# Performance work log

Measured on AMD Instinct MI355X. Metric: run time of the kernel, lower is better.

## Reference

```python
import jax, jax.numpy as jnp
import numpy as np

B = 16
Dv, Hv, Wv = 128, 128, 128   # patchsize voxel grid (C=1)
NPTS = 1920                  # 16*120 points
EPS_IN = 1e-5                # InstanceNorm eps


def _inorm(x):
    # InstanceNorm1d, affine=False: normalize over last (length) dim per (b, c)
    m = jnp.mean(x, axis=-1, keepdims=True)
    v = jnp.var(x, axis=-1, keepdims=True)
    return (x - m) * jax.lax.rsqrt(v + EPS_IN)


def _mlp(q, w1, b1, w2, b2, w3, b3, w4, b4, w5, b5):
    b = q.shape[0]
    x = q.reshape(b, 256, 8)                                    # (b, 2048//8, 8)
    x = jnp.einsum('bil,oi->bol', x, w1) + b1[None, :, None]    # Conv1d(256,240,1) -> (b,240,8)
    x = jax.nn.relu(_inorm(x.reshape(b, 64, 30)))               # view (b,64,30), IN(64)
    # Conv1d(64,128,1,groups=64): each in-ch -> 2 out-chs; then view (b,32,120)
    x = (x[:, :, None, :] * w2[None, :, :, None] + b2.reshape(1, 64, 2, 1)).reshape(b, 32, 120)
    x = jax.nn.relu(_inorm(x))
    # Conv1d(32,64,1,groups=32); view (b,16,480)
    x = (x[:, :, None, :] * w3[None, :, :, None] + b3.reshape(1, 32, 2, 1)).reshape(b, 16, 480)
    x = jax.nn.relu(_inorm(x))
    # Conv1d(16,64,1,groups=16); view (b,16,1920)
    x = (x[:, :, None, :] * w4[None, :, :, None] + b4.reshape(1, 16, 4, 1)).reshape(b, 16, 1920)
    x = jax.nn.relu(_inorm(x))
    return jnp.einsum('bil,oi->bol', x, w5) + b5[None, :, None]  # Conv1d(16,3,1) -> (b,3,1920)


def _splat(vals, grid):
    # True adjoint of 3D grid_sample (align_corners=False, zeros padding):
    # trilinear scatter-add of point values into the voxel grid.
    # vals: (b, N); grid: (b, N, 3) with (x, y, z) ~ (W, H, D) normalized coords.
    b, n = vals.shape
    px = ((grid[..., 0] + 1.0) * Wv - 1.0) * 0.5
    py = ((grid[..., 1] + 1.0) * Hv - 1.0) * 0.5
    pz = ((grid[..., 2] + 1.0) * Dv - 1.0) * 0.5
    x0f = jnp.floor(px); y0f = jnp.floor(py); z0f = jnp.floor(pz)
    fx = px - x0f; fy = py - y0f; fz = pz - z0f
    x0 = x0f.astype(jnp.int32); y0 = y0f.astype(jnp.int32); z0 = z0f.astype(jnp.int32)
    bidx = jnp.arange(b, dtype=jnp.int32)[:, None]
    out = jnp.zeros(b * Dv * Hv * Wv, dtype=vals.dtype)
    for dz in (0, 1):
        wz = fz if dz else (1.0 - fz)
        for dy in (0, 1):
            wy = fy if dy else (1.0 - fy)
            for dx in (0, 1):
                wx = fx if dx else (1.0 - fx)
                xi = x0 + dx; yi = y0 + dy; zi = z0 + dz
                w = wx * wy * wz * vals
                valid = (xi >= 0) & (xi < Wv) & (yi >= 0) & (yi < Hv) & (zi >= 0) & (zi < Dv)
                w = jnp.where(valid, w, 0.0)
                xi = jnp.clip(xi, 0, Wv - 1)
                yi = jnp.clip(yi, 0, Hv - 1)
                zi = jnp.clip(zi, 0, Dv - 1)
                flat = ((bidx * Dv + zi) * Hv + yi) * Wv + xi
                out = out.at[flat.ravel()].add(w.ravel())
    return out.reshape(b, 1, Dv, Hv, Wv)


def _avgpool3(x):
    # AvgPool3d(3, stride=1, padding=1, count_include_pad=True) as separable 1D averages
    for ax in (2, 3, 4):
        pad = [(1, 1) if i == ax else (0, 0) for i in range(5)]
        xp = jnp.pad(x, pad)
        n = x.shape[ax]
        x = (jax.lax.slice_in_dim(xp, 0, n, axis=ax)
             + jax.lax.slice_in_dim(xp, 1, n + 1, axis=ax)
             + jax.lax.slice_in_dim(xp, 2, n + 2, axis=ax)) / 3.0
    return x


def _smooth(x):
    return _avgpool3(_avgpool3(_avgpool3(x)))


def _forward(q, q_val, w1, b1, w2, b2, w3, b3, w4, b4, w5, b5):
    b = q.shape[0]
    q3 = _mlp(q, w1, b1, w2, b2, w3, b3, w4, b4, w5, b5)   # (b, 3, 1920)
    coords = jnp.tanh(q3)                                    # q0_coord
    grid = jnp.transpose(coords, (0, 2, 1))                  # (b, 1920, 3)
    vals = jnp.broadcast_to(jax.nn.sigmoid(q_val).reshape(1, NPTS), (b, NPTS))
    out = _splat(vals, grid)
    out0 = _splat(jnp.ones((b, NPTS), q.dtype), grid)
    return _smooth(out) / (_smooth(out0) + 0.001)


def setup_inputs() -> dict:
    key = jax.random.key(0)
    ks = jax.random.split(key, 12)
    sc = 0.1
    return {
        'q': jax.random.normal(ks[0], (B, 2048), jnp.float32),
        'q_val': jax.random.normal(ks[1], (1, 1, 16, 120), jnp.float32),
        'w1': jax.random.normal(ks[2], (240, 256), jnp.float32) * sc,
        'b1': jax.random.normal(ks[3], (240,), jnp.float32) * sc,
        'w2': jax.random.normal(ks[4], (64, 2), jnp.float32) * sc,
        'b2': jax.random.normal(ks[5], (128,), jnp.float32) * sc,
        'w3': jax.random.normal(ks[6], (32, 2), jnp.float32) * sc,
        'b3': jax.random.normal(ks[7], (64,), jnp.float32) * sc,
        'w4': jax.random.normal(ks[8], (16, 4), jnp.float32) * sc,
        'b4': jax.random.normal(ks[9], (64,), jnp.float32) * sc,
        'w5': jax.random.normal(ks[10], (3, 16), jnp.float32) * sc,
        'b5': jax.random.normal(ks[11], (3,), jnp.float32) * sc,
    }


def reference(q, q_val, w1, b1, w2, b2, w3, b3, w4, b4, w5, b5):
    return _forward(q, q_val, w1, b1, w2, b2, w3, b3, w4, b4, w5, b5)
```

## Files before the change

kernel.cpp:

```cpp
#include <hip/hip_runtime.h>
#include <cstddef>

#define NB 16
#define NVOX 128
#define NPT 1920
#define NPAIRS 32768

static __device__ __forceinline__ float2 f2(float a, float b) {
    float2 r; r.x = a; r.y = b; return r;
}

__global__ __launch_bounds__(256)
void zero_out(float4* __restrict__ out)
{
    int idx = blockIdx.x * 2048 + threadIdx.x;
    #pragma unroll
    for (int i = 0; i < 8; ++i)
        out[idx + i * 256] = make_float4(0.f, 0.f, 0.f, 0.f);
}

__global__ __launch_bounds__(1024)
void mega_tail(const float* __restrict__ q, const float* __restrict__ w1,
               const float* __restrict__ b1, const float* __restrict__ qval,
               const float* __restrict__ w2, const float* __restrict__ b2,
               const float* __restrict__ w3, const float* __restrict__ b3,
               const float* __restrict__ w4, const float* __restrict__ b4,
               const float* __restrict__ w5, const float* __restrict__ b5,
               float4* __restrict__ pts, int* __restrict__ count,
               int* __restrict__ list)
{
    __shared__ float qs[2048];
    __shared__ float x1s[1920];
    __shared__ float h3[16 * 480];
    __shared__ float m4s[16], r4s[16];
    __shared__ unsigned char lflags[2048];

    const int b = blockIdx.x;
    const int t = threadIdx.x;

    for (int u = t; u < 2048; u += 1024) {
        qs[u] = q[b * 2048 + u];
        lflags[u] = 0;
    }
    __syncthreads();

    for (int u = t; u < 1920; u += 1024) {
        int o = u >> 3, l = u & 7;
        const float4* wr = (const float4*)(w1 + o * 256);
        float acc = 0.f;
        #pragma unroll 8
        for (int i4 = 0; i4 < 64; ++i4) {
            float4 w = wr[i4];
            int base = i4 * 32 + l;
            acc = fmaf(w.x, qs[base],      acc);
            acc = fmaf(w.y, qs[base + 8],  acc);
            acc = fmaf(w.z, qs[base + 16], acc);
            acc = fmaf(w.w, qs[base + 24], acc);
        }
        x1s[u] = b1[o] + acc;
    }
    __syncthreads();

    const int w = t >> 6;
    const int l = t & 63;
    const int c1l = l >> 4;
    const int p16 = l & 15;
    const int c1  = 4 * w + c1l;
    const bool hasb = (p16 < 14);

    const float* xrow = x1s + c1 * 30;
    float a0 = xrow[p16];
    float a1 = hasb ? xrow[p16 + 16] : 0.f;

    float s = a0 + a1, s2 = a0 * a0 + a1 * a1;
    #pragma unroll
    for (int m = 1; m <= 8; m <<= 1) {
        s  += __shfl_xor(s,  m);
        s2 += __shfl_xor(s2, m);
    }
    float mean = s * (1.f / 30.f);
    float var  = s2 * (1.f / 30.f) - mean * mean;
    float rstd = rsqrtf(var + 1e-5f);
    a0 = fmaxf((a0 - mean) * rstd, 0.f);
    a1 = fmaxf((a1 - mean) * rstd, 0.f);

    const float w20 = w2[c1 * 2 + 0], w21 = w2[c1 * 2 + 1];
    const float b20 = b2[c1 * 2 + 0], b21 = b2[c1 * 2 + 1];
    float y00 = fmaf(a0, w20, b20), y01 = fmaf(a0, w21, b21);
    float y10 = fmaf(a1, w20, b20), y11 = fmaf(a1, w21, b21);

    float u1 = y00 + y01 + (hasb ? (y10 + y11) : 0.f);
    float u2 = y00 * y00 + y01 * y01 + (hasb ? (y10 * y10 + y11 * y11) : 0.f);
    #pragma unroll
    for (int m = 1; m <= 16; m <<= 1) {
        u1 += __shfl_xor(u1, m);
        u2 += __shfl_xor(u2, m);
    }
    mean = u1 * (1.f / 120.f);
    var  = u2 * (1.f / 120.f) - mean * mean;
    rstd = rsqrtf(var + 1e-5f);
    y00 = fmaxf((y00 - mean) * rstd, 0.f);
    y01 = fmaxf((y01 - mean) * rstd, 0.f);
    y10 = fmaxf((y10 - mean) * rstd, 0.f);
    y11 = fmaxf((y11 - mean) * rstd, 0.f);

    const int c2 = c1 >> 1;
    const float w30 = w3[c2 * 2 + 0], w31 = w3[c2 * 2 + 1];
    const float b30 = b3[c2 * 2 + 0], b31 = b3[c2 * 2 + 1];
    float z000 = fmaf(y00, w30, b30), z001 = fmaf(y00, w31, b31);
    float z010 = fmaf(y01, w30, b30), z011 = fmaf(y01, w31, b31);
    float z100 = fmaf(y10, w30, b30), z101 = fmaf(y10, w31, b31);
    float z110 = fmaf(y11, w30, b30), z111 = fmaf(y11, w31, b31);

    float v1 = z000 + z001 + z010 + z011
             + (hasb ? (z100 + z101 + z110 + z111) : 0.f);
    float v2 = z000 * z000 + z001 * z001 + z010 * z010 + z011 * z011
             + (hasb ? (z100 * z100 + z101 * z101 + z110 * z110 + z111 * z111) : 0.f);
    #pragma unroll
    for (int m = 1; m <= 32; m <<= 1) {
        v1 += __shfl_xor(v1, m);
        v2 += __shfl_xor(v2, m);
    }
    mean = v1 * (1.f / 480.f);
    var  = v2 * (1.f / 480.f) - mean * mean;
    rstd = rsqrtf(var + 1e-5f);

    const int qb0 = (c1l >> 1) * 240;
    const int pb0 = (c1l & 1) * 60;
    float* hw = h3 + w * 480;
    float s4 = 0.f, q4 = 0.f;
    {
        float v;
        v = fmaxf((z000 - mean) * rstd, 0.f); hw[qb0 +       pb0 +      p16] = v; s4 += v; q4 += v * v;
        v = fmaxf((z001 - mean) * rstd, 0.f); hw[qb0 + 120 + pb0 +      p16] = v; s4 += v; q4 += v * v;
        v = fmaxf((z010 - mean) * rstd, 0.f); hw[qb0 +       pb0 + 30 + p16] = v; s4 += v; q4 += v * v;
        v = fmaxf((z011 - mean) * rstd, 0.f); hw[qb0 + 120 + pb0 + 30 + p16] = v; s4 += v; q4 += v * v;
        if (hasb) {
            v = fmaxf((z100 - mean) * rstd, 0.f); hw[qb0 +       pb0 +      p16 + 16] = v; s4 += v; q4 += v * v;
            v = fmaxf((z101 - mean) * rstd, 0.f); hw[qb0 + 120 + pb0 +      p16 + 16] = v; s4 += v; q4 += v * v;
            v = fmaxf((z110 - mean) * rstd, 0.f); hw[qb0 +       pb0 + 30 + p16 + 16] = v; s4 += v; q4 += v * v;
            v = fmaxf((z111 - mean) * rstd, 0.f); hw[qb0 + 120 + pb0 + 30 + p16 + 16] = v; s4 += v; q4 += v * v;
        }
    }
    #pragma unroll
    for (int m = 1; m <= 32; m <<= 1) {
        s4 += __shfl_xor(s4, m);
        q4 += __shfl_xor(q4, m);
    }
    if (l == 0) {
        float sum4 = 0.f, sq4 = 0.f;
        #pragma unroll
        for (int j = 0; j < 4; ++j) {
            float ww = w4[w * 4 + j], bb = b4[w * 4 + j];
            sum4 += ww * s4 + 480.f * bb;
            sq4  += ww * ww * q4 + 2.f * ww * bb * s4 + 480.f * bb * bb;
        }
        float m4 = sum4 * (1.f / 1920.f);
        float var4 = sq4 * (1.f / 1920.f) - m4 * m4;
        m4s[w] = m4; r4s[w] = rsqrtf(var4 + 1e-5f);
    }
    __syncthreads();

    for (int p = t; p < NPT; p += 1024) {
        int j = p / 480;
        int pp = p - j * 480;
        float a0e = b5[0], a1e = b5[1], a2e = b5[2];
        #pragma unroll
        for (int c = 0; c < 16; ++c) {
            float xv = h3[c * 480 + pp];
            float x4 = fmaf(xv, w4[c * 4 + j], b4[c * 4 + j]);
            float h  = fmaxf((x4 - m4s[c]) * r4s[c], 0.f);
            a0e = fmaf(w5[c],      h, a0e);
            a1e = fmaf(w5[16 + c], h, a1e);
            a2e = fmaf(w5[32 + c], h, a2e);
        }
        float px = tanhf(a0e) * 64.f + 63.5f;
        float py = tanhf(a1e) * 64.f + 63.5f;
        float pz = tanhf(a2e) * 64.f + 63.5f;
        float val = 1.f / (1.f + expf(-qval[p]));

        float4 pv; pv.x = px; pv.y = py; pv.z = pz; pv.w = val;
        pts[b * NPT + p] = pv;

        int x0 = (int)floorf(px), y0 = (int)floorf(py), z0 = (int)floorf(pz);
        int xlo = max(0, x0 - 3), xhi = min(127, x0 + 4);
        int ylo = max(0, y0 - 3), yhi = min(127, y0 + 4);
        int zlo = max(0, z0 - 3), zhi = min(127, z0 + 4);
        if (xlo > xhi || ylo > yhi || zlo > zhi) continue;
        int pxl = xlo >> 4, pxh = xhi >> 4;
        int tyl = ylo >> 3, tyh = yhi >> 3;
        int tzl = zlo >> 3, tzh = zhi >> 3;
        for (int tz = tzl; tz <= tzh; ++tz)
            for (int ty = tyl; ty <= tyh; ++ty)
                for (int px2 = pxl; px2 <= pxh; ++px2)
                    lflags[(tz * 16 + ty) * 8 + px2] = 1;
    }
    __syncthreads();

    for (int u = t; u < 2048; u += 1024) {
        if (lflags[u]) {
            int pos = atomicAdd(count, 1);
            list[pos] = b * 2048 + u;
        }
    }
}

__device__ __forceinline__ void coef(int g, float& cm1, float& c0, float& cp1)
{
    cm1 = (g == 1 || g == 127) ? 5.f : 6.f;
    c0  = (g == 0 || g == 127) ? 4.f : 7.f;
    cp1 = (g == 0 || g == 126) ? 5.f : 6.f;
}

__global__ __launch_bounds__(512, 8)
void tile_persist(const float4* __restrict__ pts, const int* __restrict__ count,
                  const int* __restrict__ list, float* __restrict__ out)
{
    __shared__ float2 raw[14 * 14 * 22];

    const int cnt = *count;
    const int t = threadIdx.x;

    for (int idx = blockIdx.x; idx < cnt; idx += gridDim.x) {
        const int code = list[idx];
        const int pair = code & 7;
        const int ty   = (code >> 3) & 15;
        const int tz   = (code >> 7) & 15;
        const int b    = code >> 11;
        const int Tx = pair * 16, Ty = ty * 8, Tz = tz * 8;

        float* ob = out + (((size_t)(b * NVOX + Tz) * NVOX + Ty) * NVOX + Tx);

        {
            float4* rz = (float4*)raw;
            for (int u = t; u < 2156; u += 512) rz[u] = make_float4(0.f, 0.f, 0.f, 0.f);
        }
        __syncthreads();

        const float4* pb = pts + b * NPT;
        for (int p = t; p < NPT; p += 512) {
            float4 pt = pb[p];
            float x0f = floorf(pt.x), y0f = floorf(pt.y), z0f = floorf(pt.z);
            int x0 = (int)x0f, y0 = (int)y0f, z0 = (int)z0f;
            int lx0 = x0 - Tx + 3, ly0 = y0 - Ty + 3, lz0 = z0 - Tz + 3;
            if (lx0 + 1 < 0 || lx0 > 21 || ly0 + 1 < 0 || ly0 > 13 ||
                lz0 + 1 < 0 || lz0 > 13) continue;
            float fx = pt.x - x0f, fy = pt.y - y0f, fz = pt.z - z0f;
            float val = pt.w;
            #pragma unroll
            for (int dz = 0; dz < 2; ++dz) {
                int zi = z0 + dz, lz = lz0 + dz;
                if ((unsigned)zi >= 128u || (unsigned)lz >= 14u) continue;
                float wz = dz ? fz : 1.f - fz;
                #pragma unroll
                for (int dy = 0; dy < 2; ++dy) {
                    int yi = y0 + dy, ly = ly0 + dy;
                    if ((unsigned)yi >= 128u || (unsigned)ly >= 14u) continue;
                    float wy = dy ? fy : 1.f - fy;
                    #pragma unroll
                    for (int dx = 0; dx < 2; ++dx) {
                        int xi = x0 + dx, lx = lx0 + dx;
                        if ((unsigned)xi >= 128u || (unsigned)lx >= 22u) continue;
                        float w = (dx ? fx : 1.f - fx) * wy * wz;
                        float2* cell = &raw[(lz * 14 + ly) * 22 + lx];
                        atomicAdd(&cell->x, w * val);
                        atomicAdd(&cell->y, w);
                    }
                }
            }
        }
        __syncthreads();

        if (t < 308) {
            float2 w0 = raw[t],           w1 = raw[t + 308],     w2 = raw[t + 2 * 308],
                   w3 = raw[t + 3 * 308], w4 = raw[t + 4 * 308], w5 = raw[t + 5 * 308],
                   w6 = raw[t + 6 * 308];
            #pragma unroll
            for (int z = 0; z < 8; ++z) {
                float cm1, c0, cp1; coef(Tz + z, cm1, c0, cp1);
                float sx = (w0.x + w6.x) + 3.f * (w1.x + w5.x)
                         + cm1 * w2.x + c0 * w3.x + cp1 * w4.x;
                float sy = (w0.y + w6.y) + 3.f * (w1.y + w5.y)
                         + cm1 * w2.y + c0 * w3.y + cp1 * w4.y;
                float2 nxt = raw[t + ((z < 7) ? z + 7 : 7) * 308];
                raw[t + z * 308] = f2(sx * (1.f / 27.f), sy * (1.f / 27.f));
                w0 = w1; w1 = w2; w2 = w3; w3 = w4; w4 = w5; w5 = w6; w6 = nxt;
            }
        }
        __syncthreads();

        if (t < 176) {
            int z = t / 22, lx = t - z * 22;
            float2* base = &raw[z * 308 + lx];
            float2 w0 = base[0],      w1 = base[22],     w2 = base[2 * 22],
                   w3 = base[3 * 22], w4 = base[4 * 22], w5 = base[5 * 22],
                   w6 = base[6 * 22];
            #pragma unroll
            for (int y = 0; y < 8; ++y) {
                float cm1, c0, cp1; coef(Ty + y, cm1, c0, cp1);
                float sx = (w0.x + w6.x) + 3.f * (w1.x + w5.x)
                         + cm1 * w2.x + c0 * w3.x + cp1 * w4.x;
                float sy = (w0.y + w6.y) + 3.f * (w1.y + w5.y)
                         + cm1 * w2.y + c0 * w3.y + cp1 * w4.y;
                float2 nxt = base[((y < 7) ? y + 7 : 7) * 22];
                base[y * 22] = f2(sx * (1.f / 27.f), sy * (1.f / 27.f));
                w0 = w1; w1 = w2; w2 = w3; w3 = w4; w4 = w5; w5 = w6; w6 = nxt;
            }
        }
        __syncthreads();

        if (t < 128) {
            int row = t >> 1, half = t & 1;
            int z = row >> 3, y = row & 7;
            const float2* a = &raw[z * 308 + y * 22 + half * 8];
            float2 w0 = a[0], w1 = a[1], w2 = a[2], w3 = a[3],
                   w4 = a[4], w5 = a[5], w6 = a[6];
            float res[8];
            #pragma unroll
            for (int i = 0; i < 8; ++i) {
                int x = half * 8 + i;
                float cm1, c0, cp1; coef(Tx + x, cm1, c0, cp1);
                float sx = (w0.x + w6.x) + 3.f * (w1.x + w5.x)
                         + cm1 * w2.x + c0 * w3.x + cp1 * w4.x;
                float sy = (w0.y + w6.y) + 3.f * (w1.y + w5.y)
                         + cm1 * w2.y + c0 * w3.y + cp1 * w4.y;
                res[i] = (sx * (1.f / 27.f)) / (sy * (1.f / 27.f) + 0.001f);
                float2 nxt = a[(i < 7) ? i + 7 : 13];
                w0 = w1; w1 = w2; w2 = w3; w3 = w4; w4 = w5; w5 = w6; w6 = nxt;
            }
            float* orow = &ob[((size_t)z * NVOX + y) * NVOX + half * 8];
            *(float4*)&orow[0] = make_float4(res[0], res[1], res[2], res[3]);
            *(float4*)&orow[4] = make_float4(res[4], res[5], res[6], res[7]);
        }
        __syncthreads();
    }
}

extern "C" void kernel_launch(void* const* d_in, const int* in_sizes, int n_in,
                              void* d_out, int out_size, void* d_ws, size_t ws_size,
                              hipStream_t stream)
{
    const float* q    = (const float*)d_in[0];
    const float* qval = (const float*)d_in[1];
    const float* w1   = (const float*)d_in[2];
    const float* b1   = (const float*)d_in[3];
    const float* w2   = (const float*)d_in[4];
    const float* b2   = (const float*)d_in[5];
    const float* w3   = (const float*)d_in[6];
    const float* b3   = (const float*)d_in[7];
    const float* w4   = (const float*)d_in[8];
    const float* b4   = (const float*)d_in[9];
    const float* w5   = (const float*)d_in[10];
    const float* b5   = (const float*)d_in[11];
    float* out = (float*)d_out;

    int*    count = (int*)d_ws;
    int*    list  = (int*)((char*)d_ws + 16);
    float4* pts   = (float4*)((char*)d_ws + 131088);

    hipMemsetAsync(count, 0, 4, stream);

    zero_out<<<4096, 256, 0, stream>>>((float4*)out);

    mega_tail<<<NB, 1024, 0, stream>>>(q, w1, b1, qval, w2, b2, w3, b3,
                                       w4, b4, w5, b5, pts, count, list);

    tile_persist<<<1024, 512, 0, stream>>>(pts, count, list, out);
}
```

Before: 232.5 us.

## Fuse MLP tail and tile splatting into one cooperative kernel with grid sync

Merges the per-batch MLP/point-generation kernel and the persistent tile-splat kernel into a single cooperative launch separated by a grid-wide sync. Both phases share one union of shared memory. Block size drops from 1024/512 to 256 threads, and the tail work is looped over channel groups. The global atomic counter and its memset are replaced by per-batch local counts, which the tile phase prefix-walks to find work. This removes a launch and the memset, but shrinks the tail phase to 256 threads on only 16 blocks, adds grid-sync overhead, and the tile loop now has fewer threads per tile.

```diff
diff --git a/kernel.cpp b/kernel.cpp
--- a/kernel.cpp
+++ b/kernel.cpp
@@ -1,13 +1,39 @@
 #include <hip/hip_runtime.h>
+#include <hip/hip_cooperative_groups.h>
 #include <cstddef>
+
+namespace cg = cooperative_groups;
 
 #define NB 16
 #define NVOX 128
 #define NPT 1920
 #define NPAIRS 32768
 
+struct SMemA {
+    float x1s[1920];
+    float h3[7680];
+    float m4s[16], r4s[16];
+    unsigned char lflags[2048];
+    int lcount;
+};
+struct SMemB {
+    float2 raw[4312];
+    int bc[16];
+};
+union __align__(16) SMem {
+    SMemA a;
+    SMemB b;
+};
+
 static __device__ __forceinline__ float2 f2(float a, float b) {
     float2 r; r.x = a; r.y = b; return r;
+}
+
+__device__ __forceinline__ void coef(int g, float& cm1, float& c0, float& cp1)
+{
+    cm1 = (g == 1 || g == 127) ? 5.f : 6.f;
+    c0  = (g == 0 || g == 127) ? 4.f : 7.f;
+    cp1 = (g == 0 || g == 126) ? 5.f : 6.f;
 }
 
 __global__ __launch_bounds__(256)
@@ -19,32 +45,27 @@
         out[idx + i * 256] = make_float4(0.f, 0.f, 0.f, 0.f);
 }
 
-__global__ __launch_bounds__(1024)
-void mega_tail(const float* __restrict__ q, const float* __restrict__ w1,
-               const float* __restrict__ b1, const float* __restrict__ qval,
-               const float* __restrict__ w2, const float* __restrict__ b2,
-               const float* __restrict__ w3, const float* __restrict__ b3,
-               const float* __restrict__ w4, const float* __restrict__ b4,
-               const float* __restrict__ w5, const float* __restrict__ b5,
-               float4* __restrict__ pts, int* __restrict__ count,
-               int* __restrict__ list)
-{
-    __shared__ float qs[2048];
-    __shared__ float x1s[1920];
-    __shared__ float h3[16 * 480];
-    __shared__ float m4s[16], r4s[16];
-    __shared__ unsigned char lflags[2048];
-
-    const int b = blockIdx.x;
-    const int t = threadIdx.x;
-
-    for (int u = t; u < 2048; u += 1024) {
+__device__ void tail_phase(SMem* S, int b, int t,
+    const float* __restrict__ q, const float* __restrict__ w1,
+    const float* __restrict__ b1, const float* __restrict__ qval,
+    const float* __restrict__ w2, const float* __restrict__ b2,
+    const float* __restrict__ w3, const float* __restrict__ b3,
+    const float* __restrict__ w4, const float* __restrict__ b4,
+    const float* __restrict__ w5, const float* __restrict__ b5,
+    float4* __restrict__ pts, int* __restrict__ bcount,
+    int* __restrict__ list)
+{
+    SMemA* A = &S->a;
+    float* qs = A->h3;
+
+    for (int u = t; u < 2048; u += 256) {
         qs[u] = q[b * 2048 + u];
-        lflags[u] = 0;
-    }
-    __syncthreads();
-
-    for (int u = t; u < 1920; u += 1024) {
+        A->lflags[u] = 0;
+    }
+    if (t == 0) A->lcount = 0;
+    __syncthreads();
+
+    for (int u = t; u < 1920; u += 256) {
         int o = u >> 3, l = u & 7;
         const float4* wr = (const float4*)(w1 + o * 256);
         float acc = 0.f;
@@ -57,119 +78,123 @@
             acc = fmaf(w.z, qs[base + 16], acc);
             acc = fmaf(w.w, qs[base + 24], acc);
         }
-        x1s[u] = b1[o] + acc;
-    }
-    __syncthreads();
-
-    const int w = t >> 6;
+        A->x1s[u] = b1[o] + acc;
+    }
+    __syncthreads();
+
     const int l = t & 63;
     const int c1l = l >> 4;
     const int p16 = l & 15;
-    const int c1  = 4 * w + c1l;
     const bool hasb = (p16 < 14);
 
-    const float* xrow = x1s + c1 * 30;
-    float a0 = xrow[p16];
-    float a1 = hasb ? xrow[p16 + 16] : 0.f;
-
-    float s = a0 + a1, s2 = a0 * a0 + a1 * a1;
-    #pragma unroll
-    for (int m = 1; m <= 8; m <<= 1) {
-        s  += __shfl_xor(s,  m);
-        s2 += __shfl_xor(s2, m);
-    }
-    float mean = s * (1.f / 30.f);
-    float var  = s2 * (1.f / 30.f) - mean * mean;
-    float rstd = rsqrtf(var + 1e-5f);
-    a0 = fmaxf((a0 - mean) * rstd, 0.f);
-    a1 = fmaxf((a1 - mean) * rstd, 0.f);
-
-    const float w20 = w2[c1 * 2 + 0], w21 = w2[c1 * 2 + 1];
-    const float b20 = b2[c1 * 2 + 0], b21 = b2[c1 * 2 + 1];
-    float y00 = fmaf(a0, w20, b20), y01 = fmaf(a0, w21, b21);
-    float y10 = fmaf(a1, w20, b20), y11 = fmaf(a1, w21, b21);
-
-    float u1 = y00 + y01 + (hasb ? (y10 + y11) : 0.f);
-    float u2 = y00 * y00 + y01 * y01 + (hasb ? (y10 * y10 + y11 * y11) : 0.f);
-    #pragma unroll
-    for (int m = 1; m <= 16; m <<= 1) {
-        u1 += __shfl_xor(u1, m);
-        u2 += __shfl_xor(u2, m);
-    }
-    mean = u1 * (1.f / 120.f);
-    var  = u2 * (1.f / 120.f) - mean * mean;
-    rstd = rsqrtf(var + 1e-5f);
-    y00 = fmaxf((y00 - mean) * rstd, 0.f);
-    y01 = fmaxf((y01 - mean) * rstd, 0.f);
-    y10 = fmaxf((y10 - mean) * rstd, 0.f);
-    y11 = fmaxf((y11 - mean) * rstd, 0.f);
-
-    const int c2 = c1 >> 1;
-    const float w30 = w3[c2 * 2 + 0], w31 = w3[c2 * 2 + 1];
-    const float b30 = b3[c2 * 2 + 0], b31 = b3[c2 * 2 + 1];
-    float z000 = fmaf(y00, w30, b30), z001 = fmaf(y00, w31, b31);
-    float z010 = fmaf(y01, w30, b30), z011 = fmaf(y01, w31, b31);
-    float z100 = fmaf(y10, w30, b30), z101 = fmaf(y10, w31, b31);
-    float z110 = fmaf(y11, w30, b30), z111 = fmaf(y11, w31, b31);
-
-    float v1 = z000 + z001 + z010 + z011
-             + (hasb ? (z100 + z101 + z110 + z111) : 0.f);
-    float v2 = z000 * z000 + z001 * z001 + z010 * z010 + z011 * z011
-             + (hasb ? (z100 * z100 + z101 * z101 + z110 * z110 + z111 * z111) : 0.f);
-    #pragma unroll
-    for (int m = 1; m <= 32; m <<= 1) {
-        v1 += __shfl_xor(v1, m);
-        v2 += __shfl_xor(v2, m);
-    }
-    mean = v1 * (1.f / 480.f);
-    var  = v2 * (1.f / 480.f) - mean * mean;
-    rstd = rsqrtf(var + 1e-5f);
-
-    const int qb0 = (c1l >> 1) * 240;
-    const int pb0 = (c1l & 1) * 60;
-    float* hw = h3 + w * 480;
-    float s4 = 0.f, q4 = 0.f;
-    {
-        float v;
-        v = fmaxf((z000 - mean) * rstd, 0.f); hw[qb0 +       pb0 +      p16] = v; s4 += v; q4 += v * v;
-        v = fmaxf((z001 - mean) * rstd, 0.f); hw[qb0 + 120 + pb0 +      p16] = v; s4 += v; q4 += v * v;
-        v = fmaxf((z010 - mean) * rstd, 0.f); hw[qb0 +       pb0 + 30 + p16] = v; s4 += v; q4 += v * v;
-        v = fmaxf((z011 - mean) * rstd, 0.f); hw[qb0 + 120 + pb0 + 30 + p16] = v; s4 += v; q4 += v * v;
-        if (hasb) {
-            v = fmaxf((z100 - mean) * rstd, 0.f); hw[qb0 +       pb0 +      p16 + 16] = v; s4 += v; q4 += v * v;
-            v = fmaxf((z101 - mean) * rstd, 0.f); hw[qb0 + 120 + pb0 +      p16 + 16] = v; s4 += v; q4 += v * v;
-            v = fmaxf((z110 - mean) * rstd, 0.f); hw[qb0 +       pb0 + 30 + p16 + 16] = v; s4 += v; q4 += v * v;
-            v = fmaxf((z111 - mean) * rstd, 0.f); hw[qb0 + 120 + pb0 + 30 + p16 + 16] = v; s4 += v; q4 += v * v;
-        }
-    }
-    #pragma unroll
-    for (int m = 1; m <= 32; m <<= 1) {
-        s4 += __shfl_xor(s4, m);
-        q4 += __shfl_xor(q4, m);
-    }
-    if (l == 0) {
-        float sum4 = 0.f, sq4 = 0.f;
+    for (int cc = 0; cc < 4; ++cc) {
+        const int c3 = (t >> 6) + 4 * cc;
+        const int c1 = 4 * c3 + c1l;
+        const float* xrow = A->x1s + c1 * 30;
+        float a0 = xrow[p16];
+        float a1 = hasb ? xrow[p16 + 16] : 0.f;
+
+        float s = a0 + a1, s2 = a0 * a0 + a1 * a1;
         #pragma unroll
-        for (int j = 0; j < 4; ++j) {
-            float ww = w4[w * 4 + j], bb = b4[w * 4 + j];
-            sum4 += ww * s4 + 480.f * bb;
-            sq4  += ww * ww * q4 + 2.f * ww * bb * s4 + 480.f * bb * bb;
-        }
-        float m4 = sum4 * (1.f / 1920.f);
-        float var4 = sq4 * (1.f / 1920.f) - m4 * m4;
-        m4s[w] = m4; r4s[w] = rsqrtf(var4 + 1e-5f);
-    }
-    __syncthreads();
-
-    for (int p = t; p < NPT; p += 1024) {
+        for (int m = 1; m <= 8; m <<= 1) {
+            s  += __shfl_xor(s,  m);
+            s2 += __shfl_xor(s2, m);
+        }
+        float mean = s * (1.f / 30.f);
+        float var  = s2 * (1.f / 30.f) - mean * mean;
+        float rstd = rsqrtf(var + 1e-5f);
+        a0 = fmaxf((a0 - mean) * rstd, 0.f);
+        a1 = fmaxf((a1 - mean) * rstd, 0.f);
+
+        const float w20 = w2[c1 * 2 + 0], w21 = w2[c1 * 2 + 1];
+        const float b20 = b2[c1 * 2 + 0], b21 = b2[c1 * 2 + 1];
+        float y00 = fmaf(a0, w20, b20), y01 = fmaf(a0, w21, b21);
+        float y10 = fmaf(a1, w20, b20), y11 = fmaf(a1, w21, b21);
+
+        float u1 = y00 + y01 + (hasb ? (y10 + y11) : 0.f);
+        float u2 = y00 * y00 + y01 * y01
+                 + (hasb ? (y10 * y10 + y11 * y11) : 0.f);
+        #pragma unroll
+        for (int m = 1; m <= 16; m <<= 1) {
+            u1 += __shfl_xor(u1, m);
+            u2 += __shfl_xor(u2, m);
+        }
+        mean = u1 * (1.f / 120.f);
+        var  = u2 * (1.f / 120.f) - mean * mean;
+        rstd = rsqrtf(var + 1e-5f);
+        y00 = fmaxf((y00 - mean) * rstd, 0.f);
+        y01 = fmaxf((y01 - mean) * rstd, 0.f);
+        y10 = fmaxf((y10 - mean) * rstd, 0.f);
+        y11 = fmaxf((y11 - mean) * rstd, 0.f);
+
+        const int c2 = c1 >> 1;
+        const float w30 = w3[c2 * 2 + 0], w31 = w3[c2 * 2 + 1];
+        const float b30 = b3[c2 * 2 + 0], b31 = b3[c2 * 2 + 1];
+        float z000 = fmaf(y00, w30, b30), z001 = fmaf(y00, w31, b31);
+        float z010 = fmaf(y01, w30, b30), z011 = fmaf(y01, w31, b31);
+        float z100 = fmaf(y10, w30, b30), z101 = fmaf(y10, w31, b31);
+        float z110 = fmaf(y11, w30, b30), z111 = fmaf(y11, w31, b31);
+
+        float v1 = z000 + z001 + z010 + z011
+                 + (hasb ? (z100 + z101 + z110 + z111) : 0.f);
+        float v2 = z000 * z000 + z001 * z001 + z010 * z010 + z011 * z011
+                 + (hasb ? (z100 * z100 + z101 * z101
+                          + z110 * z110 + z111 * z111) : 0.f);
+        #pragma unroll
+        for (int m = 1; m <= 32; m <<= 1) {
+            v1 += __shfl_xor(v1, m);
+            v2 += __shfl_xor(v2, m);
+        }
+        mean = v1 * (1.f / 480.f);
+        var  = v2 * (1.f / 480.f) - mean * mean;
+        rstd = rsqrtf(var + 1e-5f);
+
+        const int qb0 = (c1l >> 1) * 240;
+        const int pb0 = (c1l & 1) * 60;
+        float* hw = A->h3 + c3 * 480;
+        float s4 = 0.f, q4 = 0.f;
+        {
+            float v;
+            v = fmaxf((z000 - mean) * rstd, 0.f); hw[qb0 +       pb0 +      p16] = v; s4 += v; q4 += v * v;
+            v = fmaxf((z001 - mean) * rstd, 0.f); hw[qb0 + 120 + pb0 +      p16] = v; s4 += v; q4 += v * v;
+            v = fmaxf((z010 - mean) * rstd, 0.f); hw[qb0 +       pb0 + 30 + p16] = v; s4 += v; q4 += v * v;
+            v = fmaxf((z011 - mean) * rstd, 0.f); hw[qb0 + 120 + pb0 + 30 + p16] = v; s4 += v; q4 += v * v;
+            if (hasb) {
+                v = fmaxf((z100 - mean) * rstd, 0.f); hw[qb0 +       pb0 +      p16 + 16] = v; s4 += v; q4 += v * v;
+                v = fmaxf((z101 - mean) * rstd, 0.f); hw[qb0 + 120 + pb0 +      p16 + 16] = v; s4 += v; q4 += v * v;
+                v = fmaxf((z110 - mean) * rstd, 0.f); hw[qb0 +       pb0 + 30 + p16 + 16] = v; s4 += v; q4 += v * v;
+                v = fmaxf((z111 - mean) * rstd, 0.f); hw[qb0 + 120 + pb0 + 30 + p16 + 16] = v; s4 += v; q4 += v * v;
+            }
+        }
+        #pragma unroll
+        for (int m = 1; m <= 32; m <<= 1) {
+            s4 += __shfl_xor(s4, m);
+            q4 += __shfl_xor(q4, m);
+        }
+        if (l == 0) {
+            float sum4 = 0.f, sq4 = 0.f;
+            #pragma unroll
+            for (int j = 0; j < 4; ++j) {
+                float ww = w4[c3 * 4 + j], bb = b4[c3 * 4 + j];
+                sum4 += ww * s4 + 480.f * bb;
+                sq4  += ww * ww * q4 + 2.f * ww * bb * s4 + 480.f * bb * bb;
+            }
+            float m4 = sum4 * (1.f / 1920.f);
+            float var4 = sq4 * (1.f / 1920.f) - m4 * m4;
+            A->m4s[c3] = m4; A->r4s[c3] = rsqrtf(var4 + 1e-5f);
+        }
+    }
+    __syncthreads();
+
+    for (int p = t; p < NPT; p += 256) {
         int j = p / 480;
         int pp = p - j * 480;
         float a0e = b5[0], a1e = b5[1], a2e = b5[2];
         #pragma unroll
         for (int c = 0; c < 16; ++c) {
-            float xv = h3[c * 480 + pp];
+            float xv = A->h3[c * 480 + pp];
             float x4 = fmaf(xv, w4[c * 4 + j], b4[c * 4 + j]);
-            float h  = fmaxf((x4 - m4s[c]) * r4s[c], 0.f);
+            float h  = fmaxf((x4 - A->m4s[c]) * A->r4s[c], 0.f);
             a0e = fmaf(w5[c],      h, a0e);
             a1e = fmaf(w5[16 + c], h, a1e);
             a2e = fmaf(w5[32 + c], h, a2e);
@@ -193,53 +218,54 @@
         for (int tz = tzl; tz <= tzh; ++tz)
             for (int ty = tyl; ty <= tyh; ++ty)
                 for (int px2 = pxl; px2 <= pxh; ++px2)
-                    lflags[(tz * 16 + ty) * 8 + px2] = 1;
-    }
-    __syncthreads();
-
-    for (int u = t; u < 2048; u += 1024) {
-        if (lflags[u]) {
-            int pos = atomicAdd(count, 1);
-            list[pos] = b * 2048 + u;
-        }
-    }
-}
-
-__device__ __forceinline__ void coef(int g, float& cm1, float& c0, float& cp1)
-{
-    cm1 = (g == 1 || g == 127) ? 5.f : 6.f;
-    c0  = (g == 0 || g == 127) ? 4.f : 7.f;
-    cp1 = (g == 0 || g == 126) ? 5.f : 6.f;
-}
-
-__global__ __launch_bounds__(512, 8)
-void tile_persist(const float4* __restrict__ pts, const int* __restrict__ count,
-                  const int* __restrict__ list, float* __restrict__ out)
-{
-    __shared__ float2 raw[14 * 14 * 22];
-
-    const int cnt = *count;
-    const int t = threadIdx.x;
-
-    for (int idx = blockIdx.x; idx < cnt; idx += gridDim.x) {
-        const int code = list[idx];
+                    A->lflags[(tz * 16 + ty) * 8 + px2] = 1;
+    }
+    __syncthreads();
+
+    for (int u = t; u < 2048; u += 256) {
+        if (A->lflags[u]) {
+            int pos = atomicAdd(&A->lcount, 1);
+            list[b * 2048 + pos] = (b << 11) | u;
+        }
+    }
+    __syncthreads();
+    if (t == 0) bcount[b] = A->lcount;
+}
+
+__device__ void tiles_phase(SMem* S, int t, int bid, int grid,
+    const float4* __restrict__ pts, const int* __restrict__ bcount,
+    const int* __restrict__ list, float* __restrict__ out)
+{
+    SMemB* Bm = &S->b;
+    if (t < 16) Bm->bc[t] = bcount[t];
+    __syncthreads();
+    int total = 0;
+    #pragma unroll
+    for (int i = 0; i < 16; ++i) total += Bm->bc[i];
+
+    float2* raw = Bm->raw;
+
+    for (int idx = bid; idx < total; idx += grid) {
+        int rem = idx, bb = 0;
+        #pragma unroll 1
+        for (; bb < 15; ++bb) { int c = Bm->bc[bb]; if (rem < c) break; rem -= c; }
+        const int code = list[bb * 2048 + rem];
         const int pair = code & 7;
         const int ty   = (code >> 3) & 15;
         const int tz   = (code >> 7) & 15;
-        const int b    = code >> 11;
+        const int pb_  = code >> 11;
         const int Tx = pair * 16, Ty = ty * 8, Tz = tz * 8;
-
-        float* ob = out + (((size_t)(b * NVOX + Tz) * NVOX + Ty) * NVOX + Tx);
+        float* ob = out + (((size_t)(pb_ * NVOX + Tz) * NVOX + Ty) * NVOX + Tx);
 
         {
             float4* rz = (float4*)raw;
-            for (int u = t; u < 2156; u += 512) rz[u] = make_float4(0.f, 0.f, 0.f, 0.f);
+            for (int u = t; u < 2156; u += 256) rz[u] = make_float4(0.f, 0.f, 0.f, 0.f);
         }
         __syncthreads();
 
-        const float4* pb = pts + b * NPT;
-        for (int p = t; p < NPT; p += 512) {
-            float4 pt = pb[p];
+        const float4* pbp = pts + pb_ * NPT;
+        for (int p = t; p < NPT; p += 256) {
+            float4 pt = pbp[p];
             float x0f = floorf(pt.x), y0f = floorf(pt.y), z0f = floorf(pt.z);
             int x0 = (int)x0f, y0 = (int)y0f, z0 = (int)z0f;
             int lx0 = x0 - Tx + 3, ly0 = y0 - Ty + 3, lz0 = z0 - Tz + 3;
@@ -271,20 +297,21 @@
         }
         __syncthreads();
 
-        if (t < 308) {
-            float2 w0 = raw[t],           w1 = raw[t + 308],     w2 = raw[t + 2 * 308],
-                   w3 = raw[t + 3 * 308], w4 = raw[t + 4 * 308], w5 = raw[t + 5 * 308],
-                   w6 = raw[t + 6 * 308];
+        for (int c = t; c < 308; c += 256) {
+            float2 w0 = raw[c],            w1_ = raw[c + 308],
+                   w2_ = raw[c + 2 * 308], w3_ = raw[c + 3 * 308],
+                   w4_ = raw[c + 4 * 308], w5_ = raw[c + 5 * 308],
+                   w6_ = raw[c + 6 * 308];
             #pragma unroll
             for (int z = 0; z < 8; ++z) {
                 float cm1, c0, cp1; coef(Tz + z, cm1, c0, cp1);
-                float sx = (w0.x + w6.x) + 3.f * (w1.x + w5.x)
-                         + cm1 * w2.x + c0 * w3.x + cp1 * w4.x;
-                float sy = (w0.y + w6.y) + 3.f * (w1.y + w5.y)
-                         + cm1 * w2.y + c0 * w3.y + cp1 * w4.y;
-                float2 nxt = raw[t + ((z < 7) ? z + 7 : 7) * 308];
-                raw[t + z * 308] = f2(sx * (1.f / 27.f), sy * (1.f / 27.f));
-                w0 = w1; w1 = w2; w2 = w3; w3 = w4; w4 = w5; w5 = w6; w6 = nxt;
+                float sx = (w0.x + w6_.x) + 3.f * (w1_.x + w5_.x)
+                         + cm1 * w2_.x + c0 * w3_.x + cp1 * w4_.x;
+                float sy = (w0.y + w6_.y) + 3.f * (w1_.y + w5_.y)
+                         + cm1 * w2_.y + c0 * w3_.y + cp1 * w4_.y;
+                float2 nxt = raw[c + ((z < 7) ? z + 7 : 7) * 308];
+                raw[c + z * 308] = f2(sx * (1.f / 27.f), sy * (1.f / 27.f));
+                w0 = w1_; w1_ = w2_; w2_ = w3_; w3_ = w4_; w4_ = w5_; w5_ = w6_; w6_ = nxt;
             }
         }
         __syncthreads();
@@ -292,48 +319,92 @@
         if (t < 176) {
             int z = t / 22, lx = t - z * 22;
             float2* base = &raw[z * 308 + lx];
-            float2 w0 = base[0],      w1 = base[22],     w2 = base[2 * 22],
-                   w3 = base[3 * 22], w4 = base[4 * 22], w5 = base[5 * 22],
-                   w6 = base[6 * 22];
+            float2 w0 = base[0],       w1_ = base[22],
+                   w2_ = base[2 * 22], w3_ = base[3 * 22],
+                   w4_ = base[4 * 22], w5_ = base[5 * 22],
+                   w6_ = base[6 * 22];
             #pragma unroll
             for (int y = 0; y < 8; ++y) {
                 float cm1, c0, cp1; coef(Ty + y, cm1, c0, cp1);
-                float sx = (w0.x + w6.x) + 3.f * (w1.x + w5.x)
-                         + cm1 * w2.x + c0 * w3.x + cp1 * w4.x;
-                float sy = (w0.y + w6.y) + 3.f * (w1.y + w5.y)
-                         + cm1 * w2.y + c0 * w3.y + cp1 * w4.y;
+                float sx = (w0.x + w6_.x) + 3.f * (w1_.x + w5_.x)
+                         + cm1 * w2_.x + c0 * w3_.x + cp1 * w4_.x;
+                float sy = (w0.y + w6_.y) + 3.f * (w1_.y + w5_.y)
+                         + cm1 * w2_.y + c0 * w3_.y + cp1 * w4_.y;
                 float2 nxt = base[((y < 7) ? y + 7 : 7) * 22];
                 base[y * 22] = f2(sx * (1.f / 27.f), sy * (1.f / 27.f));
-                w0 = w1; w1 = w2; w2 = w3; w3 = w4; w4 = w5; w5 = w6; w6 = nxt;
+                w0 = w1_; w1_ = w2_; w2_ = w3_; w3_ = w4_; w4_ = w5_; w5_ = w6_; w6_ = nxt;
             }
         }
         __syncthreads();
 
         if (t < 128) {
-            int row = t >> 1, half = t & 1;
+            int row = t >> 1, hx = t & 1;
             int z = row >> 3, y = row & 7;
-            const float2* a = &raw[z * 308 + y * 22 + half * 8];
-            float2 w0 = a[0], w1 = a[1], w2 = a[2], w3 = a[3],
-                   w4 = a[4], w5 = a[5], w6 = a[6];
+            const float2* a = &raw[z * 308 + y * 22 + hx * 8];
+            float2 w0 = a[0], w1_ = a[1], w2_ = a[2], w3_ = a[3],
+                   w4_ = a[4], w5_ = a[5], w6_ = a[6];
             float res[8];
             #pragma unroll
             for (int i = 0; i < 8; ++i) {
-                int x = half * 8 + i;
+                int x = hx * 8 + i;
                 float cm1, c0, cp1; coef(Tx + x, cm1, c0, cp1);
-                float sx = (w0.x + w6.x) + 3.f * (w1.x + w5.x)
-                         + cm1 * w2.x + c0 * w3.x + cp1 * w4.x;
-                float sy = (w0.y + w6.y) + 3.f * (w1.y + w5.y)
-                         + cm1 * w2.y + c0 * w3.y + cp1 * w4.y;
+                float sx = (w0.x + w6_.x) + 3.f * (w1_.x + w5_.x)
+                         + cm1 * w2_.x + c0 * w3_.x + cp1 * w4_.x;
+                float sy = (w0.y + w6_.y) + 3.f * (w1_.y + w5_.y)
+                         + cm1 * w2_.y + c0 * w3_.y + cp1 * w4_.y;
                 res[i] = (sx * (1.f / 27.f)) / (sy * (1.f / 27.f) + 0.001f);
                 float2 nxt = a[(i < 7) ? i + 7 : 13];
-                w0 = w1; w1 = w2; w2 = w3; w3 = w4; w4 = w5; w5 = w6; w6 = nxt;
-            }
-            float* orow = &ob[((size_t)z * NVOX + y) * NVOX + half * 8];
+                w0 = w1_; w1_ = w2_; w2_ = w3_; w3_ = w4_; w4_ = w5_; w5_ = w6_; w6_ = nxt;
+            }
+            float* orow = &ob[((size_t)z * NVOX + y) * NVOX + hx * 8];
             *(float4*)&orow[0] = make_float4(res[0], res[1], res[2], res[3]);
             *(float4*)&orow[4] = make_float4(res[4], res[5], res[6], res[7]);
         }
         __syncthreads();
     }
+}
+
+#define TAIL_ARGS const float* __restrict__ q, const float* __restrict__ w1,  \
+    const float* __restrict__ b1, const float* __restrict__ qval,             \
+    const float* __restrict__ w2, const float* __restrict__ b2,               \
+    const float* __restrict__ w3, const float* __restrict__ b3,               \
+    const float* __restrict__ w4, const float* __restrict__ b4,               \
+    const float* __restrict__ w5, const float* __restrict__ b5,               \
+    float4* __restrict__ pts, int* __restrict__ bcount,                       \
+    int* __restrict__ list
+
+__global__ __launch_bounds__(256, 4)
+void mega(TAIL_ARGS, float* __restrict__ out)
+{
+    __shared__ SMem sm;
+    const int bid = blockIdx.x;
+    const int t = threadIdx.x;
+
+    if (bid < NB)
+        tail_phase(&sm, bid, t, q, w1, b1, qval, w2, b2, w3, b3,
+                   w4, b4, w5, b5, pts, bcount, list);
+
+    __threadfence();
+    cg::this_grid().sync();
+    __threadfence();
+
+    tiles_phase(&sm, t, bid, gridDim.x, pts, bcount, list, out);
+}
+
+__global__ __launch_bounds__(256, 4)
+void tail_k(TAIL_ARGS)
+{
+    __shared__ SMem sm;
+    tail_phase(&sm, blockIdx.x, threadIdx.x, q, w1, b1, qval, w2, b2,
+               w3, b3, w4, b4, w5, b5, pts, bcount, list);
+}
+
+__global__ __launch_bounds__(256, 4)
+void tile_k(const float4* __restrict__ pts, const int* __restrict__ bcount,
+            const int* __restrict__ list, float* __restrict__ out)
+{
+    __shared__ SMem sm;
+    tiles_phase(&sm, threadIdx.x, blockIdx.x, gridDim.x, pts, bcount, list, out);
 }
 
 extern "C" void kernel_launch(void* const* d_in, const int* in_sizes, int n_in,
@@ -354,16 +425,30 @@
     const float* b5   = (const float*)d_in[11];
     float* out = (float*)d_out;
 
-    int*    count = (int*)d_ws;
-    int*    list  = (int*)((char*)d_ws + 16);
-    float4* pts   = (float4*)((char*)d_ws + 131088);
-
-    hipMemsetAsync(count, 0, 4, stream);
+    int*    bcount = (int*)d_ws;
+    int*    list   = (int*)((char*)d_ws + 64);
+    float4* pts    = (float4*)((char*)d_ws + 131136);
 
     zero_out<<<4096, 256, 0, stream>>>((float4*)out);
 
-    mega_tail<<<NB, 1024, 0, stream>>>(q, w1, b1, qval, w2, b2, w3, b3,
-                                       w4, b4, w5, b5, pts, count, list);
-
-    tile_persist<<<1024, 512, 0, stream>>>(pts, count, list, out);
-}
+    bool coop_ok = false;
+    int occ = 0;
+    if (hipOccupancyMaxActiveBlocksPerMultiprocessor(
+            &occ, (const void*)mega, 256, 0) == hipSuccess && occ > 0) {
+        int nblk = occ * 256;
+        if (nblk > 1024) nblk = 1024;
+        if (nblk >= NB) {
+            void* args[] = { &q, &w1, &b1, &qval, &w2, &b2, &w3, &b3,
+                             &w4, &b4, &w5, &b5, &pts, &bcount, &list, &out };
+            coop_ok = (hipLaunchCooperativeKernel((const void*)mega,
+                           dim3(nblk), dim3(256), args, 0, stream)
+                       == hipSuccess);
+        }
+    }
+
+    if (!coop_ok) {
+        tail_k<<<NB, 256, 0, stream>>>(q, w1, b1, qval, w2, b2, w3, b3,
+                                       w4, b4, w5, b5, pts, bcount, list);
+        tile_k<<<1024, 256, 0, stream>>>(pts, bcount, list, out);
+    }
+}
```

Measured after the change: 492.3 us. 2.12x slower.
